# Kernel tuning notes

Measured on AMD Instinct MI355X. Metric: run time of the kernel, lower is better.

## Reference

```python
import jax, jax.numpy as jnp
import numpy as np

TAU = 0.05
LAMBDA0 = 1.0
DELTA = 1.0
MU = 0.4

B, D, C = 128, 1024, 32768


def setup_inputs() -> dict:
    key = jax.random.key(0)
    k1, k2, k3 = jax.random.split(key, 3)
    inputs = jax.random.normal(k1, (B, D), jnp.float32)
    inputs = inputs / jnp.linalg.norm(inputs, axis=1, keepdims=True)  # L2-normed features
    em = jax.random.normal(k2, (C, D), jnp.float32)
    em = em / jnp.linalg.norm(em, axis=1, keepdims=True)  # memory bank rows are unit-norm
    targets = jax.random.randint(k3, (B,), 0, C, dtype=jnp.int32)
    return {"inputs": inputs, "em": em, "targets": targets, "epoch": 10}


def _adaptive_selection(scores, targets):
    # scores are detached in the original (inputs.detach().clone())
    s = jax.lax.stop_gradient(scores)
    onehot = (s > LAMBDA0 / TAU).astype(jnp.float32)      # [B, C]
    ks1 = onehot.sum(axis=1)                              # raw neighbor counts (returned)
    mask = (ks1 > 1).astype(jnp.float32)
    k = ks1 * mask + (1.0 - mask) * 2.0
    k = DELTA / (k * jnp.log(k))
    k = (k * mask)[:, None]                               # [B, 1]
    t = onehot * k
    t = t.at[jnp.arange(t.shape[0]), targets].set(1.0)    # scatter 1 at ground-truth class
    return t, ks1


def reference(inputs, em, targets, epoch):
    mu = min(MU / 60.0 * (epoch + 1), 1.0)
    scores = (inputs @ em.T) / TAU                        # [B, C]

    # epoch > 4 path: target_loss with adaptive selection
    targets_line, ks = _adaptive_selection(scores, targets)
    logp = jax.nn.log_softmax(scores, axis=1)
    loss = (-(targets_line * logp).sum(axis=1)).mean()

    # sequential per-sample EMA scatter update with renorm (original does this in backward)
    def step(mem, xy):
        x, y = xy
        row = mu * mem[y] + (1.0 - mu) * x
        row = row / jnp.linalg.norm(row)
        return mem.at[y].set(row), None

    new_em, _ = jax.lax.scan(step, em, (inputs, targets))
    return loss, ks, new_em
```

## Files before the change

### kernel.cpp

```cpp
#include <hip/hip_runtime.h>
#include <math.h>

#define BN 128
#define DN 1024
#define CN 32768
#define NCHUNK 512

__global__ __launch_bounds__(256)
void k1_gemm_stats(const float* __restrict__ inp, const float* __restrict__ em,
                   float* __restrict__ out_loss, float* __restrict__ out_em,
                   float* __restrict__ ws)
{
    __shared__ float As[32][132];
    __shared__ float Bs[32][68];
    const int t   = threadIdx.x;
    const int blk = blockIdx.x;
    const int c0  = blk * 64;
    if (blk == 0 && t == 0) out_loss[0] = 0.0f;
    const int ty = t >> 4, tx = t & 15;

    float acc[8][4];
#pragma unroll
    for (int r = 0; r < 8; ++r)
#pragma unroll
        for (int c = 0; c < 4; ++c) acc[r][c] = 0.0f;

    for (int kt = 0; kt < DN; kt += 32) {
#pragma unroll
        for (int p = 0; p < 4; ++p) {
            int q = p * 256 + t;
            int row = q >> 3, kc4 = q & 7;
            float4 v = *(const float4*)&inp[(size_t)row * DN + kt + kc4 * 4];
            As[kc4 * 4 + 0][row] = v.x;
            As[kc4 * 4 + 1][row] = v.y;
            As[kc4 * 4 + 2][row] = v.z;
            As[kc4 * 4 + 3][row] = v.w;
        }
#pragma unroll
        for (int p = 0; p < 2; ++p) {
            int q = p * 256 + t;
            int r = q >> 3, kc4 = q & 7;
            size_t gidx = (size_t)(c0 + r) * DN + kt + kc4 * 4;
            const float4 v = *(const float4*)&em[gidx];
            *(float4*)&out_em[gidx] = v;
            Bs[kc4 * 4 + 0][r] = v.x;
            Bs[kc4 * 4 + 1][r] = v.y;
            Bs[kc4 * 4 + 2][r] = v.z;
            Bs[kc4 * 4 + 3][r] = v.w;
        }
        __syncthreads();
#pragma unroll
        for (int kk = 0; kk < 32; ++kk) {
            float a[8], b[4];
            *(float4*)&a[0] = *(const float4*)&As[kk][ty * 8];
            *(float4*)&a[4] = *(const float4*)&As[kk][ty * 8 + 4];
            *(float4*)&b[0] = *(const float4*)&Bs[kk][tx * 4];
#pragma unroll
            for (int r = 0; r < 8; ++r)
#pragma unroll
                for (int c = 0; c < 4; ++c)
                    acc[r][c] = fmaf(a[r], b[c], acc[r][c]);
        }
        __syncthreads();
    }

#pragma unroll
    for (int r = 0; r < 8; ++r) {
        const int i = ty * 8 + r;
        float s[4];
#pragma unroll
        for (int c = 0; c < 4; ++c) s[c] = acc[r][c] * 20.0f;
        float m = fmaxf(fmaxf(s[0], s[1]), fmaxf(s[2], s[3]));
#pragma unroll
        for (int off = 1; off < 16; off <<= 1) m = fmaxf(m, __shfl_xor(m, off));
        float z = 0.f, cnt = 0.f, ss = 0.f;
#pragma unroll
        for (int c = 0; c < 4; ++c) {
            z += expf(s[c] - m);
            if (s[c] > 20.0f) { cnt += 1.0f; ss += s[c]; }
        }
#pragma unroll
        for (int off = 1; off < 16; off <<= 1) {
            z   += __shfl_xor(z, off);
            cnt += __shfl_xor(cnt, off);
            ss  += __shfl_xor(ss, off);
        }
        if (tx == 0) {
            float4 w = make_float4(m, z, cnt, ss);
            *(float4*)&ws[((size_t)i * NCHUNK + blk) * 4] = w;
        }
    }
}

__global__ __launch_bounds__(256)
void k2_finalize(const float* __restrict__ inp, const float* __restrict__ em,
                 const int* __restrict__ tgt, const float* __restrict__ ws,
                 float* __restrict__ d_loss, float* __restrict__ d_ks)
{
    const int i = blockIdx.x;
    const int t = threadIdx.x;
    const int wid = t >> 6, lane = t & 63;
    __shared__ float red[4][4];
    __shared__ float dred[4];

    float m = -INFINITY, z = 0.f, cnt = 0.f, ss = 0.f;
    for (int c = t; c < NCHUNK; c += 256) {
        float4 w = *(const float4*)&ws[((size_t)i * NCHUNK + c) * 4];
        float M = fmaxf(m, w.x);
        z = z * expf(m - M) + w.y * expf(w.x - M);
        m = M;
        cnt += w.z; ss += w.w;
    }
#pragma unroll
    for (int off = 1; off < 64; off <<= 1) {
        float m2 = __shfl_xor(m, off), z2 = __shfl_xor(z, off);
        float M = fmaxf(m, m2);
        z = z * expf(m - M) + z2 * expf(m2 - M);
        m = M;
        cnt += __shfl_xor(cnt, off);
        ss  += __shfl_xor(ss, off);
    }
    if (lane == 0) { red[wid][0] = m; red[wid][1] = z; red[wid][2] = cnt; red[wid][3] = ss; }

    const int y = tgt[i];
    float4 a = *(const float4*)&inp[(size_t)i * DN + t * 4];
    float4 b = *(const float4*)&em[(size_t)y * DN + t * 4];
    float d = a.x * b.x + a.y * b.y + a.z * b.z + a.w * b.w;
#pragma unroll
    for (int off = 1; off < 64; off <<= 1) d += __shfl_xor(d, off);
    if (lane == 0) dred[wid] = d;
    __syncthreads();

    if (t == 0) {
        float M = red[0][0], Z = red[0][1], CNT = red[0][2], SS = red[0][3];
#pragma unroll
        for (int w = 1; w < 4; ++w) {
            float m2 = red[w][0], z2 = red[w][1];
            float Mn = fmaxf(M, m2);
            Z = Z * expf(M - Mn) + z2 * expf(m2 - Mn);
            M = Mn; CNT += red[w][2]; SS += red[w][3];
        }
        float sy  = (dred[0] + dred[1] + dred[2] + dred[3]) * 20.0f;
        float lse = M + logf(Z);
        float A   = SS - CNT * lse;
        float ki  = (CNT > 1.0f) ? (1.0f / (CNT * logf(CNT))) : 0.0f;
        float sum_t = ki * (A - ((sy > 20.0f) ? (sy - lse) : 0.0f)) + (sy - lse);
        atomicAdd(d_loss, -sum_t * (1.0f / 128.0f));
        d_ks[i] = CNT;
    }
}

__global__ __launch_bounds__(256)
void k3_ema(const float* __restrict__ inp, const int* __restrict__ tgt,
            const void* __restrict__ epoch_p, float* __restrict__ out_em)
{
    const int j = blockIdx.x;
    const int y = tgt[j];
    for (int p = 0; p < j; ++p)
        if (tgt[p] == y) return;

    int ei = *(const int*)epoch_p;
    float e = (ei >= 0 && ei < 1000000) ? (float)ei : *(const float*)epoch_p;
    const float mu = fminf(0.4f / 60.0f * (e + 1.0f), 1.0f);
    const float om = 1.0f - mu;

    const int t = threadIdx.x;
    const int wid = t >> 6, lane = t & 63;
    __shared__ float nred[4];

    float4 r = *(const float4*)&out_em[(size_t)y * DN + t * 4];
    for (int p = j; p < BN; ++p) {
        if (tgt[p] != y) continue;
        float4 x = *(const float4*)&inp[(size_t)p * DN + t * 4];
        r.x = mu * r.x + om * x.x;
        r.y = mu * r.y + om * x.y;
        r.z = mu * r.z + om * x.z;
        r.w = mu * r.w + om * x.w;
        float n = r.x * r.x + r.y * r.y + r.z * r.z + r.w * r.w;
#pragma unroll
        for (int off = 1; off < 64; off <<= 1) n += __shfl_xor(n, off);
        if (lane == 0) nred[wid] = n;
        __syncthreads();
        n = nred[0] + nred[1] + nred[2] + nred[3];
        float inv = 1.0f / sqrtf(n);
        r.x *= inv; r.y *= inv; r.z *= inv; r.w *= inv;
        __syncthreads();
    }
    *(float4*)&out_em[(size_t)y * DN + t * 4] = r;
}

extern "C" void kernel_launch(void* const* d_in, const int* in_sizes, int n_in,
                              void* d_out, int out_size, void* d_ws, size_t ws_size,
                              hipStream_t stream)
{
    const float* inp = (const float*)d_in[0];
    const float* em  = (const float*)d_in[1];
    const int*   tgt = (const int*)d_in[2];
    const void*  ep  = d_in[3];

    float* loss   = (float*)d_out;
    float* ks     = loss + 1;
    float* out_em = ks + BN;
    float* ws     = (float*)d_ws;

    k1_gemm_stats<<<512, 256, 0, stream>>>(inp, em, loss, out_em, ws);
    k2_finalize<<<128, 256, 0, stream>>>(inp, em, tgt, ws, loss, ks);
    k3_ema<<<128, 256, 0, stream>>>(inp, tgt, ep, out_em);
}
```

Baseline: 426.1 us.

## Use bf16 MFMA for score GEMM with double-buffered register prefetch

Replaces the FP32 FMA outer-product GEMM in the first kernel with bf16 MFMA 16x16x32 instructions. Operands are converted to bf16 when staged into double-buffered LDS, and the next K tile is prefetched into registers while the current one computes. Per-block softmax statistics are now merged in shared memory across the four waves, and fast __expf replaces expf. The cost is reduced precision in the scores, which are scaled by 20 and then thresholded, so the neighbour counts near the threshold and the loss could shift slightly.

Result: faster. 343.5 us (-19.4%).

```diff
diff --git a/kernel.cpp b/kernel.cpp
--- a/kernel.cpp
+++ b/kernel.cpp
@@ -4,91 +4,134 @@
 #define BN 128
 #define DN 1024
 #define CN 32768
-#define NCHUNK 512
+#define NB 64
+#define KS 32
+#define NBLK (CN / NB)
+#define LDA 40
+
+typedef float f32x4 __attribute__((ext_vector_type(4)));
+typedef short short8 __attribute__((ext_vector_type(8)));
+
+static __device__ inline unsigned short f2b(float f) {
+    union { float f; unsigned u; } v; v.f = f;
+    unsigned r = v.u + 0x7FFF + ((v.u >> 16) & 1);
+    return (unsigned short)(r >> 16);
+}
 
 __global__ __launch_bounds__(256)
 void k1_gemm_stats(const float* __restrict__ inp, const float* __restrict__ em,
                    float* __restrict__ out_loss, float* __restrict__ out_em,
                    float* __restrict__ ws)
 {
-    __shared__ float As[32][132];
-    __shared__ float Bs[32][68];
+    __shared__ unsigned short Ab[2][BN * LDA];
+    __shared__ unsigned short Bb[2][NB * LDA];
+    __shared__ float4 smp[BN][4];
+
     const int t   = threadIdx.x;
     const int blk = blockIdx.x;
-    const int c0  = blk * 64;
+    const size_t c0 = (size_t)blk * NB;
     if (blk == 0 && t == 0) out_loss[0] = 0.0f;
-    const int ty = t >> 4, tx = t & 15;
-
-    float acc[8][4];
-#pragma unroll
-    for (int r = 0; r < 8; ++r)
-#pragma unroll
-        for (int c = 0; c < 4; ++c) acc[r][c] = 0.0f;
-
-    for (int kt = 0; kt < DN; kt += 32) {
-#pragma unroll
-        for (int p = 0; p < 4; ++p) {
-            int q = p * 256 + t;
-            int row = q >> 3, kc4 = q & 7;
-            float4 v = *(const float4*)&inp[(size_t)row * DN + kt + kc4 * 4];
-            As[kc4 * 4 + 0][row] = v.x;
-            As[kc4 * 4 + 1][row] = v.y;
-            As[kc4 * 4 + 2][row] = v.z;
-            As[kc4 * 4 + 3][row] = v.w;
+
+    const int w  = t >> 6;
+    const int l  = t & 63;
+    const int lr = l & 15, lq = l >> 4;
+
+    f32x4 acc[8];
+#pragma unroll
+    for (int m = 0; m < 8; ++m) acc[m] = (f32x4)0.0f;
+
+    const int arow[4] = { (0*256 + t) >> 3, (1*256 + t) >> 3, (2*256 + t) >> 3, (3*256 + t) >> 3 };
+    const int ak4     = t & 7;
+    const int bcol[2] = { (0*256 + t) >> 3, (1*256 + t) >> 3 };
+
+    float4 ga0[4], gb0[2], ga1[4], gb1[2];
+
+#define LOADG(kt, GA, GB)                                                         \
+    {                                                                             \
+        _Pragma("unroll")                                                         \
+        for (int p = 0; p < 4; ++p)                                               \
+            GA[p] = *(const float4*)&inp[(size_t)arow[p] * DN + (kt) + ak4 * 4];  \
+        _Pragma("unroll")                                                         \
+        for (int p = 0; p < 2; ++p)                                               \
+            GB[p] = *(const float4*)&em[(c0 + bcol[p]) * DN + (kt) + ak4 * 4];    \
+    }
+
+#define STAGE(buf, kt, GA, GB)                                                    \
+    {                                                                             \
+        _Pragma("unroll")                                                         \
+        for (int p = 0; p < 4; ++p) {                                             \
+            uint2 u;                                                              \
+            u.x = (unsigned)f2b(GA[p].x) | ((unsigned)f2b(GA[p].y) << 16);        \
+            u.y = (unsigned)f2b(GA[p].z) | ((unsigned)f2b(GA[p].w) << 16);        \
+            *(uint2*)&Ab[buf][arow[p] * LDA + ak4 * 4] = u;                       \
+        }                                                                         \
+        _Pragma("unroll")                                                         \
+        for (int p = 0; p < 2; ++p) {                                             \
+            uint2 u;                                                              \
+            u.x = (unsigned)f2b(GB[p].x) | ((unsigned)f2b(GB[p].y) << 16);        \
+            u.y = (unsigned)f2b(GB[p].z) | ((unsigned)f2b(GB[p].w) << 16);        \
+            *(uint2*)&Bb[buf][bcol[p] * LDA + ak4 * 4] = u;                       \
+            *(float4*)&out_em[(c0 + bcol[p]) * DN + (kt) + ak4 * 4] = GB[p];      \
+        }                                                                         \
+    }
+
+#define COMPUTE(buf)                                                              \
+    {                                                                             \
+        const short8 bf = *(const short8*)&Bb[buf][(w * 16 + lr) * LDA + lq * 8]; \
+        _Pragma("unroll")                                                         \
+        for (int m = 0; m < 8; ++m) {                                             \
+            const short8 af = *(const short8*)&Ab[buf][(m * 16 + lr) * LDA + lq * 8]; \
+            acc[m] = __builtin_amdgcn_mfma_f32_16x16x32_bf16(af, bf, acc[m], 0, 0, 0); \
+        }                                                                         \
+    }
+
+    LOADG(0, ga0, gb0)
+    for (int kt = 0; kt < DN; kt += 2 * KS) {
+        STAGE(0, kt, ga0, gb0)
+        __syncthreads();
+        LOADG(kt + KS, ga1, gb1)
+        COMPUTE(0)
+
+        STAGE(1, kt + KS, ga1, gb1)
+        __syncthreads();
+        if (kt + 2 * KS < DN) LOADG(kt + 2 * KS, ga0, gb0)
+        COMPUTE(1)
+    }
+    __syncthreads();
+
+#pragma unroll
+    for (int m = 0; m < 8; ++m) {
+#pragma unroll
+        for (int r = 0; r < 4; ++r) {
+            float s = acc[m][r] * 20.0f;
+            float mx = s;
+#pragma unroll
+            for (int off = 1; off < 16; off <<= 1) mx = fmaxf(mx, __shfl_xor(mx, off));
+            float z   = __expf(s - mx);
+            float cnt = (s > 20.0f) ? 1.0f : 0.0f;
+            float ss  = (s > 20.0f) ? s : 0.0f;
+#pragma unroll
+            for (int off = 1; off < 16; off <<= 1) {
+                z   += __shfl_xor(z, off);
+                cnt += __shfl_xor(cnt, off);
+                ss  += __shfl_xor(ss, off);
+            }
+            if (lr == 0) smp[m * 16 + lq * 4 + r][w] = make_float4(mx, z, cnt, ss);
         }
-#pragma unroll
-        for (int p = 0; p < 2; ++p) {
-            int q = p * 256 + t;
-            int r = q >> 3, kc4 = q & 7;
-            size_t gidx = (size_t)(c0 + r) * DN + kt + kc4 * 4;
-            const float4 v = *(const float4*)&em[gidx];
-            *(float4*)&out_em[gidx] = v;
-            Bs[kc4 * 4 + 0][r] = v.x;
-            Bs[kc4 * 4 + 1][r] = v.y;
-            Bs[kc4 * 4 + 2][r] = v.z;
-            Bs[kc4 * 4 + 3][r] = v.w;
+    }
+    __syncthreads();
+
+    if (t < BN) {
+        float4 p0 = smp[t][0];
+        float M = p0.x, Z = p0.y, CNT = p0.z, SS = p0.w;
+#pragma unroll
+        for (int q = 1; q < 4; ++q) {
+            float4 p = smp[t][q];
+            float Mn = fmaxf(M, p.x);
+            Z = Z * __expf(M - Mn) + p.y * __expf(p.x - Mn);
+            M = Mn; CNT += p.z; SS += p.w;
         }
-        __syncthreads();
-#pragma unroll
-        for (int kk = 0; kk < 32; ++kk) {
-            float a[8], b[4];
-            *(float4*)&a[0] = *(const float4*)&As[kk][ty * 8];
-            *(float4*)&a[4] = *(const float4*)&As[kk][ty * 8 + 4];
-            *(float4*)&b[0] = *(const float4*)&Bs[kk][tx * 4];
-#pragma unroll
-            for (int r = 0; r < 8; ++r)
-#pragma unroll
-                for (int c = 0; c < 4; ++c)
-                    acc[r][c] = fmaf(a[r], b[c], acc[r][c]);
-        }
-        __syncthreads();
-    }
-
-#pragma unroll
-    for (int r = 0; r < 8; ++r) {
-        const int i = ty * 8 + r;
-        float s[4];
-#pragma unroll
-        for (int c = 0; c < 4; ++c) s[c] = acc[r][c] * 20.0f;
-        float m = fmaxf(fmaxf(s[0], s[1]), fmaxf(s[2], s[3]));
-#pragma unroll
-        for (int off = 1; off < 16; off <<= 1) m = fmaxf(m, __shfl_xor(m, off));
-        float z = 0.f, cnt = 0.f, ss = 0.f;
-#pragma unroll
-        for (int c = 0; c < 4; ++c) {
-            z += expf(s[c] - m);
-            if (s[c] > 20.0f) { cnt += 1.0f; ss += s[c]; }
-        }
-#pragma unroll
-        for (int off = 1; off < 16; off <<= 1) {
-            z   += __shfl_xor(z, off);
-            cnt += __shfl_xor(cnt, off);
-            ss  += __shfl_xor(ss, off);
-        }
-        if (tx == 0) {
-            float4 w = make_float4(m, z, cnt, ss);
-            *(float4*)&ws[((size_t)i * NCHUNK + blk) * 4] = w;
-        }
+        ((float4*)ws)[(size_t)t * NBLK + blk] = make_float4(M, Z, CNT, SS);
     }
 }
 
@@ -104,18 +147,17 @@
     __shared__ float dred[4];
 
     float m = -INFINITY, z = 0.f, cnt = 0.f, ss = 0.f;
-    for (int c = t; c < NCHUNK; c += 256) {
-        float4 w = *(const float4*)&ws[((size_t)i * NCHUNK + c) * 4];
-        float M = fmaxf(m, w.x);
-        z = z * expf(m - M) + w.y * expf(w.x - M);
-        m = M;
-        cnt += w.z; ss += w.w;
+    for (int c = t; c < NBLK; c += 256) {
+        float4 wv = ((const float4*)ws)[(size_t)i * NBLK + c];
+        float M = fmaxf(m, wv.x);
+        z = z * __expf(m - M) + wv.y * __expf(wv.x - M);
+        m = M; cnt += wv.z; ss += wv.w;
     }
 #pragma unroll
     for (int off = 1; off < 64; off <<= 1) {
         float m2 = __shfl_xor(m, off), z2 = __shfl_xor(z, off);
         float M = fmaxf(m, m2);
-        z = z * expf(m - M) + z2 * expf(m2 - M);
+        z = z * __expf(m - M) + z2 * __expf(m2 - M);
         m = M;
         cnt += __shfl_xor(cnt, off);
         ss  += __shfl_xor(ss, off);
@@ -134,11 +176,11 @@
     if (t == 0) {
         float M = red[0][0], Z = red[0][1], CNT = red[0][2], SS = red[0][3];
 #pragma unroll
-        for (int w = 1; w < 4; ++w) {
-            float m2 = red[w][0], z2 = red[w][1];
+        for (int q = 1; q < 4; ++q) {
+            float m2 = red[q][0], z2 = red[q][1];
             float Mn = fmaxf(M, m2);
-            Z = Z * expf(M - Mn) + z2 * expf(m2 - Mn);
-            M = Mn; CNT += red[w][2]; SS += red[w][3];
+            Z = Z * __expf(M - Mn) + z2 * __expf(m2 - Mn);
+            M = Mn; CNT += red[q][2]; SS += red[q][3];
         }
         float sy  = (dred[0] + dred[1] + dred[2] + dred[3]) * 20.0f;
         float lse = M + logf(Z);
@@ -203,7 +245,7 @@
     float* out_em = ks + BN;
     float* ws     = (float*)d_ws;
 
-    k1_gemm_stats<<<512, 256, 0, stream>>>(inp, em, loss, out_em, ws);
-    k2_finalize<<<128, 256, 0, stream>>>(inp, em, tgt, ws, loss, ks);
-    k3_ema<<<128, 256, 0, stream>>>(inp, tgt, ep, out_em);
-}
+    k1_gemm_stats<<<NBLK, 256, 0, stream>>>(inp, em, loss, out_em, ws);
+    k2_finalize<<<BN, 256, 0, stream>>>(inp, em, tgt, ws, loss, ks);
+    k3_ema<<<BN, 256, 0, stream>>>(inp, tgt, ep, out_em);
+}
```
